# Kernel tuning notes

Measured on AMD Instinct MI355X. Metric: run time of the kernel, lower is better.

Reference implementation:

```python
import jax, jax.numpy as jnp
import numpy as np

N_NODES = 50000
N_EDGES = 400000
N_GRAPHS = 64
D_IN = 256
D_HID = 256
D_OUT = 16


def _gcn_conv(x, edge_index, W, b):
    """PyG-style GCNConv: h = D^{-1/2}(A+I)D^{-1/2} (x @ W) + b."""
    n = x.shape[0]
    loop = jnp.arange(n)
    src = jnp.concatenate([edge_index[0], loop])  # [E+N]
    dst = jnp.concatenate([edge_index[1], loop])
    deg = jax.ops.segment_sum(jnp.ones_like(dst, x.dtype), dst, num_segments=n)
    dinv = jnp.where(deg > 0, jax.lax.rsqrt(deg), jnp.zeros_like(deg))
    norm = dinv[src] * dinv[dst]  # [E+N]
    h = x @ W  # linear transform first (as PyG does)
    msg = h[src] * norm[:, None]  # gather + scale, [E+N, D]
    out = jax.ops.segment_sum(msg, dst, num_segments=n)  # scatter-add
    return out + b


def setup_inputs() -> dict:
    key = jax.random.key(0)
    ks = jax.random.split(key, 12)
    x = jax.random.normal(ks[0], (N_NODES, D_IN), dtype=jnp.float32)
    edge_index = jax.random.randint(ks[1], (2, N_EDGES), 0, N_NODES, dtype=jnp.int64)
    batch = jnp.sort(jax.random.randint(ks[2], (N_NODES,), 0, N_GRAPHS, dtype=jnp.int64))

    def glorot(k, fan_in, fan_out):
        s = np.sqrt(6.0 / (fan_in + fan_out)).astype(np.float32)
        return jax.random.uniform(k, (fan_in, fan_out), jnp.float32, -s, s)

    return {
        "x": x,
        "edge_index": edge_index,
        "batch": batch,
        "W1": glorot(ks[3], D_IN, D_HID), "b1": jnp.zeros((D_HID,), jnp.float32),
        "W2": glorot(ks[4], D_HID, D_HID), "b2": jnp.zeros((D_HID,), jnp.float32),
        "W3": glorot(ks[5], D_HID, D_HID), "b3": jnp.zeros((D_HID,), jnp.float32),
        "Wfc": glorot(ks[6], D_HID, D_OUT), "bfc": jnp.zeros((D_OUT,), jnp.float32),
    }


def reference(x, edge_index, batch, W1, b1, W2, b2, W3, b3, Wfc, bfc):
    h = jax.nn.relu(_gcn_conv(x, edge_index, W1, b1))
    h = jax.nn.relu(_gcn_conv(h, edge_index, W2, b2))
    h = jax.nn.relu(_gcn_conv(h, edge_index, W3, b3))
    # global_mean_pool over batch ids
    sums = jax.ops.segment_sum(h, batch, num_segments=N_GRAPHS)  # [G, D]
    cnts = jax.ops.segment_sum(jnp.ones_like(batch, h.dtype), batch, num_segments=N_GRAPHS)
    pooled = sums / jnp.maximum(cnts, 1.0)[:, None]
    return pooled @ Wfc + bfc  # [G, D_OUT]
```

## Files before the change

### kernel.cpp

```cpp
#include <hip/hip_runtime.h>

#define NN 50000
#define NE 400000
#define NG 64
#define D 256
#define DOUT 16

typedef __attribute__((ext_vector_type(8))) _Float16 f16x8;
typedef __attribute__((ext_vector_type(8))) unsigned short u16x8;
typedef __attribute__((ext_vector_type(4))) float f32x4;

__device__ __forceinline__ unsigned short f2h(float x) {
    union { _Float16 h; unsigned short u; } v;
    v.h = (_Float16)x;
    return v.u;
}
__device__ __forceinline__ float h2f(unsigned short u) {
    union { _Float16 h; unsigned short u; } v;
    v.u = u;
    return (float)v.h;
}

__device__ __forceinline__ void async_cp16(void* lds, const void* g) {
    __builtin_amdgcn_global_load_lds(
        (const __attribute__((address_space(1))) unsigned int*)g,
        (__attribute__((address_space(3))) unsigned int*)lds, 16, 0, 0);
}


__global__ void k_init(int* __restrict__ cnt, float* __restrict__ pooled,
                       const int* __restrict__ batch, float* __restrict__ inv_cnt,
                       int n) {
    int i = blockIdx.x * 256 + threadIdx.x;
    if (i < n) cnt[i] = 0;
    if (i < NG * D) pooled[i] = 0.f;
    if (blockIdx.x == 0 && threadIdx.x < NG) {
        int g = threadIdx.x;
        int lo = 0, hi = n;
        while (lo < hi) { int mid = (lo + hi) >> 1; if (batch[mid] < g) lo = mid + 1; else hi = mid; }
        int start = lo;
        hi = n;
        while (lo < hi) { int mid = (lo + hi) >> 1; if (batch[mid] < g + 1) lo = mid + 1; else hi = mid; }
        inv_cnt[g] = 1.f / fmaxf((float)(lo - start), 1.f);
    }
}


__global__ void k_split_count(const float* __restrict__ x, unsigned short* __restrict__ ahi,
                              int total4, int xblocks,
                              const float* __restrict__ W1, short* __restrict__ w1h,
                              const float* __restrict__ W2, short* __restrict__ w2h,
                              const float* __restrict__ W3, short* __restrict__ w3h,
                              const int* __restrict__ eidx, int* __restrict__ cnt, int E) {
    int b = blockIdx.x;
    if (b < xblocks) {
        int i = b * 256 + threadIdx.x;
        if (i >= total4) return;
        float4 v = ((const float4*)x)[i];
        ushort4 h;
        h.x = f2h(v.x);
        h.y = f2h(v.y);
        h.z = f2h(v.z);
        h.w = f2h(v.w);
        ((ushort4*)ahi)[i] = h;
    } else if (b < xblocks + 3 * 256) {
        int wb = b - xblocks;
        int which = wb >> 8;
        int idx = (wb & 255) * 256 + threadIdx.x;
        int nn = idx >> 8, k = idx & 255;
        const float* W = (which == 0) ? W1 : (which == 1) ? W2 : W3;
        short* Wh = (which == 0) ? w1h : (which == 1) ? w2h : w3h;
        Wh[idx] = (short)f2h(W[k * 256 + nn]);
    } else {
        int e = (b - xblocks - 3 * 256) * 256 + threadIdx.x;
        if (e < E) atomicAdd(&cnt[eidx[E + e]], 1);
    }
}

__global__ void k_scan1(const int* __restrict__ cnt, int* __restrict__ excl,
                        int* __restrict__ bsums, float* __restrict__ dinv, int n) {
    __shared__ int sh[256];
    int tid = threadIdx.x;
    int base = blockIdx.x * 1024;
    int v[4]; int tsum = 0;
    for (int j = 0; j < 4; ++j) {
        int i = base + tid * 4 + j;
        v[j] = (i < n) ? cnt[i] : 0;
        if (i < n) dinv[i] = rsqrtf((float)(v[j] + 1));
        tsum += v[j];
    }
    sh[tid] = tsum; __syncthreads();
    for (int d = 1; d < 256; d <<= 1) {
        int t = (tid >= d) ? sh[tid - d] : 0;
        __syncthreads();
        sh[tid] += t;
        __syncthreads();
    }
    int run = sh[tid] - tsum;
    for (int j = 0; j < 4; ++j) {
        int i = base + tid * 4 + j;
        if (i < n) excl[i] = run;
        run += v[j];
    }
    if (tid == 255) bsums[blockIdx.x] = sh[255];
}

__global__ void k_scan3(int* __restrict__ row_ptr, const int* __restrict__ bsums,
                        int* __restrict__ cursor, int n, int E, int nb) {
    __shared__ int off_s;
    int chunk = (int)(blockIdx.x >> 2);
    if (threadIdx.x < 64) {
        int v = ((int)threadIdx.x < nb && (int)threadIdx.x < chunk) ? bsums[threadIdx.x] : 0;
        #pragma unroll
        for (int d = 1; d < 64; d <<= 1) v += __shfl_xor(v, d);
        if (threadIdx.x == 0) off_s = v;
    }
    __syncthreads();
    int off = off_s;
    int i = blockIdx.x * 256 + threadIdx.x;
    if (i < n) {
        int v = row_ptr[i] + off;
        row_ptr[i] = v;
        cursor[i] = v;
    }
    if (i == 0) row_ptr[n] = E;
}


__device__ __forceinline__ void gemm_body(
        const unsigned short* __restrict__ A,
        const short* __restrict__ Wh,
        const float* __restrict__ dinv, unsigned short* __restrict__ C, int M,
        int bm, short* Ah_s, short* Bh_s) {
    const int tid = threadIdx.x;
    const int lane = tid & 63;
    const int w    = tid >> 6;
    const int lm   = lane & 15;
    const int quad = lane >> 4;

    const int srow = tid >> 3, c = tid & 7;
    const int q = c ^ ((srow >> 1) & 7);
    const unsigned short* pa[2];
    #pragma unroll
    for (int j = 0; j < 2; ++j) {
        int ga = bm + j * 32 + srow; if (ga >= M) ga = M - 1;
        pa[j] = A + ((size_t)ga << 8) + q * 8;
    }
    const short* pbh[8];
    #pragma unroll
    for (int j = 0; j < 8; ++j)
        pbh[j] = Wh + ((size_t)(j * 32 + srow) << 8) + q * 8;

    int st[8];
    #pragma unroll
    for (int j = 0; j < 8; ++j) st[j] = j * 2048 + w * 512;

    int oa[4], ob[4];
    #pragma unroll
    for (int i = 0; i < 4; ++i) {
        int ra = i * 16 + lm;
        oa[i] = ra * 64 + ((quad ^ ((ra >> 1) & 7)) * 8);
        int rb = w * 64 + i * 16 + lm;
        ob[i] = rb * 64 + ((quad ^ ((rb >> 1) & 7)) * 8);
    }

    f32x4 acc[4][4];
    #pragma unroll
    for (int i = 0; i < 4; ++i)
        #pragma unroll
        for (int j = 0; j < 4; ++j)
            acc[i][j] = (f32x4){0.f, 0.f, 0.f, 0.f};

    for (int k0 = 0; k0 < D; k0 += 64) {
        #pragma unroll
        for (int j = 0; j < 2; ++j) async_cp16(&Ah_s[st[j]], pa[j] + k0);
        #pragma unroll
        for (int j = 0; j < 8; ++j) async_cp16(&Bh_s[st[j]], pbh[j] + k0);
        __syncthreads();

        #pragma unroll
        for (int kh = 0; kh < 2; ++kh) {
            const int xo = kh * 32;
            f16x8 Ah[4], Bh[4];
            #pragma unroll
            for (int i = 0; i < 4; ++i) {
                Ah[i] = *(const f16x8*)&Ah_s[oa[i] ^ xo];
                Bh[i] = *(const f16x8*)&Bh_s[ob[i] ^ xo];
            }
            #pragma unroll
            for (int mi = 0; mi < 4; ++mi)
                #pragma unroll
                for (int ni = 0; ni < 4; ++ni)
                    acc[mi][ni] = __builtin_amdgcn_mfma_f32_16x16x32_f16(Ah[mi], Bh[ni], acc[mi][ni], 0, 0, 0);
        }
        __syncthreads();
    }

    #pragma unroll
    for (int mi = 0; mi < 4; ++mi) {
        int rbase = bm + mi * 16 + quad * 4;
        #pragma unroll
        for (int r = 0; r < 4; ++r) {
            int grow = rbase + r;
            if (grow < M) {
                float s = dinv[grow];
                #pragma unroll
                for (int ni = 0; ni < 4; ++ni) {
                    int col = w * 64 + ni * 16 + lm;
                    C[(size_t)grow * D + col] = f2h(acc[mi][ni][r] * s);
                }
            }
        }
    }
}

__global__ __launch_bounds__(256, 3) void k_gemm_mfma(
        const unsigned short* __restrict__ A,
        const short* __restrict__ Wh,
        const float* __restrict__ dinv, unsigned short* __restrict__ C, int M) {
    __shared__ short Ah_s[4096];
    __shared__ short Bh_s[16384];
    gemm_body(A, Wh, dinv, C, M, blockIdx.x * 64, Ah_s, Bh_s);
}

__global__ __launch_bounds__(256, 3) void k_gemm1_fill(
        const unsigned short* __restrict__ A,
        const short* __restrict__ Wh,
        const float* __restrict__ dinv, unsigned short* __restrict__ C, int M,
        int gblocks, const int* __restrict__ eidx, int* __restrict__ cursor,
        int* __restrict__ col_src, int E) {
    __shared__ short Ah_s[4096];
    __shared__ short Bh_s[16384];
    if ((int)blockIdx.x < gblocks) {
        gemm_body(A, Wh, dinv, C, M, blockIdx.x * 64, Ah_s, Bh_s);
    } else {
        int e = ((int)blockIdx.x - gblocks) * 256 + threadIdx.x;
        if (e < E) {
            int d = eidx[E + e];
            int pos = atomicAdd(&cursor[d], 1);
            col_src[pos] = eidx[e];
        }
    }
}


__global__ __launch_bounds__(256) void k_agg(
        const unsigned short* __restrict__ h, const float* __restrict__ dinv,
        const int* __restrict__ row_ptr, const int* __restrict__ col_src,
        const float* __restrict__ bias,
        unsigned short* __restrict__ ohi, int n) {
    int w = threadIdx.x >> 6, lane = threadIdx.x & 63;
    int node = blockIdx.x * 4 + w;
    if (node >= n) return;
    int half = lane >> 5;
    int dcol = lane & 31;

    float acc[8] = {0.f, 0.f, 0.f, 0.f, 0.f, 0.f, 0.f, 0.f};
    if (half == 0) {
        u16x8 sv = ((const u16x8*)(h + (size_t)node * D))[dcol];
        #pragma unroll
        for (int d = 0; d < 8; ++d) acc[d] = h2f(sv[d]);
    }

    int beg = row_ptr[node], end = row_ptr[node + 1];
    for (int c = beg; c < end; c += 64) {
        int cnt = min(64, end - c);
        int myidx = (lane < cnt) ? col_src[c + lane] : 0;
        for (int e = 0; e < cnt; e += 16) {
            u16x8 u[8];
            bool val[8];
            #pragma unroll
            for (int j = 0; j < 8; ++j) {
                int eid = e + j * 2 + half;
                val[j] = eid < cnt;
                if (val[j]) {
                    int s = __shfl(myidx, eid);
                    u[j] = ((const u16x8*)(h + (size_t)s * D))[dcol];
                }
            }
            #pragma unroll
            for (int j = 0; j < 8; ++j)
                if (val[j]) {
                    #pragma unroll
                    for (int d = 0; d < 8; ++d) acc[d] += h2f(u[j][d]);
                }
        }
    }

    #pragma unroll
    for (int d = 0; d < 8; ++d) acc[d] += __shfl_xor(acc[d], 32);

    if (half == 0) {
        float di = dinv[node];
        float4 b0 = ((const float4*)bias)[dcol * 2];
        float4 b1 = ((const float4*)bias)[dcol * 2 + 1];
        float bb[8] = {b0.x, b0.y, b0.z, b0.w, b1.x, b1.y, b1.z, b1.w};
        u16x8 o;
        #pragma unroll
        for (int d = 0; d < 8; ++d)
            o[d] = f2h(fmaxf(acc[d] * di + bb[d], 0.f));
        ((u16x8*)(ohi + (size_t)node * D))[dcol] = o;
    }
}


__global__ __launch_bounds__(256) void k_pool_sum(
        const unsigned short* __restrict__ hi,
        const int* __restrict__ batch, float* __restrict__ pooled, int n) {
    int beg = blockIdx.x * 64;
    if (beg >= n) return;
    int end = min(beg + 64, n);
    int t = threadIdx.x;
    float acc = 0.f;
    int cur = batch[beg];
    for (int i = beg; i < end; ++i) {
        int g = batch[i];
        if (g != cur) {
            atomicAdd(&pooled[cur * D + t], acc);
            acc = 0.f;
            cur = g;
        }
        acc += h2f(hi[(size_t)i * D + t]);
    }
    atomicAdd(&pooled[cur * D + t], acc);
}


__global__ void k_fc(const float* __restrict__ pooled, const float* __restrict__ inv_cnt,
                     const float* __restrict__ W, const float* __restrict__ b,
                     float* __restrict__ out) {
    int t = blockIdx.x * blockDim.x + threadIdx.x;
    if (t >= NG * DOUT) return;
    int g = t >> 4, o = t & 15;
    float acc = 0.f;
    for (int k = 0; k < D; ++k) acc += pooled[g * D + k] * W[k * DOUT + o];
    out[t] = acc * inv_cnt[g] + b[o];
}


extern "C" void kernel_launch(void* const* d_in, const int* in_sizes, int n_in,
                              void* d_out, int out_size, void* d_ws, size_t ws_size,
                              hipStream_t stream) {
    const float* x    = (const float*)d_in[0];
    const int*   eidx = (const int*)d_in[1];
    const int*   batch= (const int*)d_in[2];
    const float* W1   = (const float*)d_in[3];
    const float* b1   = (const float*)d_in[4];
    const float* W2   = (const float*)d_in[5];
    const float* b2   = (const float*)d_in[6];
    const float* W3   = (const float*)d_in[7];
    const float* b3   = (const float*)d_in[8];
    const float* Wfc  = (const float*)d_in[9];
    const float* bfc  = (const float*)d_in[10];
    float* out = (float*)d_out;

    const int n = in_sizes[0] / D;
    const int E = in_sizes[1] / 2;

    char* p = (char*)d_ws;
    auto take = [&](size_t bytes) -> void* {
        void* q = (void*)p;
        p += (bytes + 255) & ~(size_t)255;
        return q;
    };
    int*   cnt     = (int*)take((size_t)n * 4);
    int*   row_ptr = (int*)take((size_t)(n + 1) * 4);
    int*   cursor  = (int*)take((size_t)n * 4);
    int*   col_src = (int*)take((size_t)E * 4);
    int*   bsums   = (int*)take(256 * 4);
    float* dinv    = (float*)take((size_t)n * 4);
    float* inv_cnt = (float*)take((size_t)NG * 4);
    short* w1h     = (short*)take((size_t)D * D * 2);
    short* w2h     = (short*)take((size_t)D * D * 2);
    short* w3h     = (short*)take((size_t)D * D * 2);
    unsigned short* hbuf = (unsigned short*)take((size_t)n * D * 2);
    unsigned short* ahi  = (unsigned short*)take((size_t)n * D * 2);
    float* pooled  = (float*)take((size_t)NG * D * 4);

    int tb = 256;
    int gn = (n + tb - 1) / tb;
    int ge = (E + tb - 1) / tb;
    int nb = (n + 1023) / 1024;
    int total4 = n * D / 4;
    int xblocks = (total4 + 255) / 256;

    k_init<<<gn, tb, 0, stream>>>(cnt, pooled, batch, inv_cnt, n);
    k_split_count<<<xblocks + 3 * 256 + ge, tb, 0, stream>>>(
        x, ahi, total4, xblocks,
        W1, w1h, W2, w2h, W3, w3h,
        eidx, cnt, E);
    k_scan1<<<nb, 256, 0, stream>>>(cnt, row_ptr, bsums, dinv, n);
    k_scan3<<<gn, tb, 0, stream>>>(row_ptr, bsums, cursor, n, E, nb);

    int ggrid = (n + 63) / 64;
    int agrid = (n + 3) / 4;

    k_gemm1_fill<<<ggrid + ge, 256, 0, stream>>>(ahi, w1h, dinv, hbuf, n,
                                                 ggrid, eidx, cursor, col_src, E);
    k_agg<<<agrid, 256, 0, stream>>>(hbuf, dinv, row_ptr, col_src, b1, ahi, n);

    k_gemm_mfma<<<ggrid, 256, 0, stream>>>(ahi, w2h, dinv, hbuf, n);
    k_agg<<<agrid, 256, 0, stream>>>(hbuf, dinv, row_ptr, col_src, b2, ahi, n);

    k_gemm_mfma<<<ggrid, 256, 0, stream>>>(ahi, w3h, dinv, hbuf, n);
    k_agg<<<agrid, 256, 0, stream>>>(hbuf, dinv, row_ptr, col_src, b3, ahi, n);

    k_pool_sum<<<(n + 63) / 64, 256, 0, stream>>>(ahi, batch, pooled, n);
    k_fc<<<4, 256, 0, stream>>>(pooled, inv_cnt, Wfc, bfc, out);
}
```

Before: 349.2 us.

## Load GEMM MFMA operands directly from global memory, dropping LDS staging

The GEMM body no longer copies A and W tiles into shared memory through async global-to-LDS loads with barriers. Each lane now reads its f16x8 MFMA fragments straight from global memory at each 32-wide k step, and the loop is fully unrolled. This removes the LDS traffic, the swizzle arithmetic and the __syncthreads, and frees LDS so more blocks can be resident. In exchange, the W tile is fetched redundantly by every wave and block through the caches, and the per-lane 16-byte loads are scattered across rows.

```diff
diff --git a/kernel.cpp b/kernel.cpp
--- a/kernel.cpp
+++ b/kernel.cpp
@@ -19,12 +19,6 @@
     union { _Float16 h; unsigned short u; } v;
     v.u = u;
     return (float)v.h;
-}
-
-__device__ __forceinline__ void async_cp16(void* lds, const void* g) {
-    __builtin_amdgcn_global_load_lds(
-        (const __attribute__((address_space(1))) unsigned int*)g,
-        (__attribute__((address_space(3))) unsigned int*)lds, 16, 0, 0);
 }
 
 
@@ -131,37 +125,21 @@
         const unsigned short* __restrict__ A,
         const short* __restrict__ Wh,
         const float* __restrict__ dinv, unsigned short* __restrict__ C, int M,
-        int bm, short* Ah_s, short* Bh_s) {
+        int bm) {
     const int tid = threadIdx.x;
     const int lane = tid & 63;
     const int w    = tid >> 6;
     const int lm   = lane & 15;
     const int quad = lane >> 4;
 
-    const int srow = tid >> 3, c = tid & 7;
-    const int q = c ^ ((srow >> 1) & 7);
-    const unsigned short* pa[2];
-    #pragma unroll
-    for (int j = 0; j < 2; ++j) {
-        int ga = bm + j * 32 + srow; if (ga >= M) ga = M - 1;
-        pa[j] = A + ((size_t)ga << 8) + q * 8;
-    }
-    const short* pbh[8];
-    #pragma unroll
-    for (int j = 0; j < 8; ++j)
-        pbh[j] = Wh + ((size_t)(j * 32 + srow) << 8) + q * 8;
-
-    int st[8];
-    #pragma unroll
-    for (int j = 0; j < 8; ++j) st[j] = j * 2048 + w * 512;
-
-    int oa[4], ob[4];
+    const unsigned short* pa[4];
+    const short* pb[4];
     #pragma unroll
     for (int i = 0; i < 4; ++i) {
-        int ra = i * 16 + lm;
-        oa[i] = ra * 64 + ((quad ^ ((ra >> 1) & 7)) * 8);
-        int rb = w * 64 + i * 16 + lm;
-        ob[i] = rb * 64 + ((quad ^ ((rb >> 1) & 7)) * 8);
+        int ra = bm + i * 16 + lm; if (ra >= M) ra = M - 1;
+        pa[i] = A + ((size_t)ra << 8) + quad * 8;
+        int cb = w * 64 + i * 16 + lm;
+        pb[i] = Wh + ((size_t)cb << 8) + quad * 8;
     }
 
     f32x4 acc[4][4];
@@ -171,29 +149,19 @@
         for (int j = 0; j < 4; ++j)
             acc[i][j] = (f32x4){0.f, 0.f, 0.f, 0.f};
 
-    for (int k0 = 0; k0 < D; k0 += 64) {
-        #pragma unroll
-        for (int j = 0; j < 2; ++j) async_cp16(&Ah_s[st[j]], pa[j] + k0);
-        #pragma unroll
-        for (int j = 0; j < 8; ++j) async_cp16(&Bh_s[st[j]], pbh[j] + k0);
-        __syncthreads();
-
-        #pragma unroll
-        for (int kh = 0; kh < 2; ++kh) {
-            const int xo = kh * 32;
-            f16x8 Ah[4], Bh[4];
+    #pragma unroll
+    for (int k0 = 0; k0 < D; k0 += 32) {
+        f16x8 Ah[4], Bh[4];
+        #pragma unroll
+        for (int i = 0; i < 4; ++i) {
+            Ah[i] = *(const f16x8*)(pa[i] + k0);
+            Bh[i] = *(const f16x8*)(pb[i] + k0);
+        }
+        #pragma unroll
+        for (int mi = 0; mi < 4; ++mi)
             #pragma unroll
-            for (int i = 0; i < 4; ++i) {
-                Ah[i] = *(const f16x8*)&Ah_s[oa[i] ^ xo];
-                Bh[i] = *(const f16x8*)&Bh_s[ob[i] ^ xo];
-            }
-            #pragma unroll
-            for (int mi = 0; mi < 4; ++mi)
-                #pragma unroll
-                for (int ni = 0; ni < 4; ++ni)
-                    acc[mi][ni] = __builtin_amdgcn_mfma_f32_16x16x32_f16(Ah[mi], Bh[ni], acc[mi][ni], 0, 0, 0);
-        }
-        __syncthreads();
+            for (int ni = 0; ni < 4; ++ni)
+                acc[mi][ni] = __builtin_amdgcn_mfma_f32_16x16x32_f16(Ah[mi], Bh[ni], acc[mi][ni], 0, 0, 0);
     }
 
     #pragma unroll
@@ -218,9 +186,7 @@
         const unsigned short* __restrict__ A,
         const short* __restrict__ Wh,
         const float* __restrict__ dinv, unsigned short* __restrict__ C, int M) {
-    __shared__ short Ah_s[4096];
-    __shared__ short Bh_s[16384];
-    gemm_body(A, Wh, dinv, C, M, blockIdx.x * 64, Ah_s, Bh_s);
+    gemm_body(A, Wh, dinv, C, M, blockIdx.x * 64);
 }
 
 __global__ __launch_bounds__(256, 3) void k_gemm1_fill(
@@ -229,10 +195,8 @@
         const float* __restrict__ dinv, unsigned short* __restrict__ C, int M,
         int gblocks, const int* __restrict__ eidx, int* __restrict__ cursor,
         int* __restrict__ col_src, int E) {
-    __shared__ short Ah_s[4096];
-    __shared__ short Bh_s[16384];
     if ((int)blockIdx.x < gblocks) {
-        gemm_body(A, Wh, dinv, C, M, blockIdx.x * 64, Ah_s, Bh_s);
+        gemm_body(A, Wh, dinv, C, M, blockIdx.x * 64);
     } else {
         int e = ((int)blockIdx.x - gblocks) * 256 + threadIdx.x;
         if (e < E) {
```

Result: slower. 400.7 us (+14.8%).

## Aggregate two nodes per wavefront and raise GEMM occupancy hint

Applied to the files above, without the earlier changes.

The aggregation kernel now processes two destination nodes per wavefront, interleaving their neighbor gathers in the same loop so more independent loads are in flight per wave, and halves the grid size. GEMM kernels' launch bounds go from 3 to 4 waves per EU, constraining registers for higher occupancy. The paired gather doubles register use for accumulators and loaded vectors and may cause imbalance when the two nodes have different degrees. The tighter register cap on the GEMM risks spills.

```diff
diff --git a/kernel.cpp b/kernel.cpp
--- a/kernel.cpp
+++ b/kernel.cpp
@@ -214,7 +214,7 @@
     }
 }
 
-__global__ __launch_bounds__(256, 3) void k_gemm_mfma(
+__global__ __launch_bounds__(256, 4) void k_gemm_mfma(
         const unsigned short* __restrict__ A,
         const short* __restrict__ Wh,
         const float* __restrict__ dinv, unsigned short* __restrict__ C, int M) {
@@ -223,7 +223,7 @@
     gemm_body(A, Wh, dinv, C, M, blockIdx.x * 64, Ah_s, Bh_s);
 }
 
-__global__ __launch_bounds__(256, 3) void k_gemm1_fill(
+__global__ __launch_bounds__(256, 4) void k_gemm1_fill(
         const unsigned short* __restrict__ A,
         const short* __restrict__ Wh,
         const float* __restrict__ dinv, unsigned short* __restrict__ C, int M,
@@ -250,56 +250,91 @@
         const float* __restrict__ bias,
         unsigned short* __restrict__ ohi, int n) {
     int w = threadIdx.x >> 6, lane = threadIdx.x & 63;
-    int node = blockIdx.x * 4 + w;
-    if (node >= n) return;
+    int node0 = (blockIdx.x * 4 + w) * 2;
+    if (node0 >= n) return;
+    bool two = (node0 + 1) < n;
     int half = lane >> 5;
     int dcol = lane & 31;
 
-    float acc[8] = {0.f, 0.f, 0.f, 0.f, 0.f, 0.f, 0.f, 0.f};
+    float a0[8] = {0.f, 0.f, 0.f, 0.f, 0.f, 0.f, 0.f, 0.f};
+    float a1[8] = {0.f, 0.f, 0.f, 0.f, 0.f, 0.f, 0.f, 0.f};
     if (half == 0) {
-        u16x8 sv = ((const u16x8*)(h + (size_t)node * D))[dcol];
-        #pragma unroll
-        for (int d = 0; d < 8; ++d) acc[d] = h2f(sv[d]);
-    }
-
-    int beg = row_ptr[node], end = row_ptr[node + 1];
-    for (int c = beg; c < end; c += 64) {
-        int cnt = min(64, end - c);
-        int myidx = (lane < cnt) ? col_src[c + lane] : 0;
-        for (int e = 0; e < cnt; e += 16) {
-            u16x8 u[8];
-            bool val[8];
+        u16x8 sv = ((const u16x8*)(h + (size_t)node0 * D))[dcol];
+        #pragma unroll
+        for (int d = 0; d < 8; ++d) a0[d] = h2f(sv[d]);
+    } else if (two) {
+        u16x8 sv = ((const u16x8*)(h + (size_t)(node0 + 1) * D))[dcol];
+        #pragma unroll
+        for (int d = 0; d < 8; ++d) a1[d] = h2f(sv[d]);
+    }
+
+    int c0 = row_ptr[node0];
+    int end0 = row_ptr[node0 + 1];
+    int c1 = end0;
+    int end1 = two ? row_ptr[node0 + 2] : end0;
+
+    while (c0 < end0 || c1 < end1) {
+        int cnt0 = min(64, end0 - c0); if (cnt0 < 0) cnt0 = 0;
+        int cnt1 = min(64, end1 - c1); if (cnt1 < 0) cnt1 = 0;
+        int my0 = (lane < cnt0) ? col_src[c0 + lane] : 0;
+        int my1 = (lane < cnt1) ? col_src[c1 + lane] : 0;
+        int mx = max(cnt0, cnt1);
+        for (int e = 0; e < mx; e += 16) {
+            u16x8 u0[8], u1[8];
+            bool v0[8], v1[8];
             #pragma unroll
             for (int j = 0; j < 8; ++j) {
                 int eid = e + j * 2 + half;
-                val[j] = eid < cnt;
-                if (val[j]) {
-                    int s = __shfl(myidx, eid);
-                    u[j] = ((const u16x8*)(h + (size_t)s * D))[dcol];
+                v0[j] = eid < cnt0;
+                if (v0[j]) {
+                    int s = __shfl(my0, eid);
+                    u0[j] = ((const u16x8*)(h + (size_t)s * D))[dcol];
+                }
+                v1[j] = eid < cnt1;
+                if (v1[j]) {
+                    int s = __shfl(my1, eid);
+                    u1[j] = ((const u16x8*)(h + (size_t)s * D))[dcol];
                 }
             }
             #pragma unroll
-            for (int j = 0; j < 8; ++j)
-                if (val[j]) {
+            for (int j = 0; j < 8; ++j) {
+                if (v0[j]) {
                     #pragma unroll
-                    for (int d = 0; d < 8; ++d) acc[d] += h2f(u[j][d]);
+                    for (int d = 0; d < 8; ++d) a0[d] += h2f(u0[j][d]);
                 }
+                if (v1[j]) {
+                    #pragma unroll
+                    for (int d = 0; d < 8; ++d) a1[d] += h2f(u1[j][d]);
+                }
+            }
         }
-    }
-
-    #pragma unroll
-    for (int d = 0; d < 8; ++d) acc[d] += __shfl_xor(acc[d], 32);
-
+        c0 += cnt0;
+        c1 += cnt1;
+    }
+
+    #pragma unroll
+    for (int d = 0; d < 8; ++d) {
+        a0[d] += __shfl_xor(a0[d], 32);
+        a1[d] += __shfl_xor(a1[d], 32);
+    }
+
+    float4 b0 = ((const float4*)bias)[dcol * 2];
+    float4 b1 = ((const float4*)bias)[dcol * 2 + 1];
+    float bb[8] = {b0.x, b0.y, b0.z, b0.w, b1.x, b1.y, b1.z, b1.w};
     if (half == 0) {
-        float di = dinv[node];
-        float4 b0 = ((const float4*)bias)[dcol * 2];
-        float4 b1 = ((const float4*)bias)[dcol * 2 + 1];
-        float bb[8] = {b0.x, b0.y, b0.z, b0.w, b1.x, b1.y, b1.z, b1.w};
+        float di = dinv[node0];
         u16x8 o;
         #pragma unroll
         for (int d = 0; d < 8; ++d)
-            o[d] = f2h(fmaxf(acc[d] * di + bb[d], 0.f));
-        ((u16x8*)(ohi + (size_t)node * D))[dcol] = o;
+            o[d] = f2h(fmaxf(a0[d] * di + bb[d], 0.f));
+        ((u16x8*)(ohi + (size_t)node0 * D))[dcol] = o;
+    } else if (two) {
+        float di = dinv[node0 + 1];
+        u16x8 o;
+        #pragma unroll
+        for (int d = 0; d < 8; ++d)
+            o[d] = f2h(fmaxf(a1[d] * di + bb[d], 0.f));
+        ((u16x8*)(ohi + (size_t)(node0 + 1) * D))[dcol] = o;
     }
 }
 
@@ -393,7 +428,7 @@
     k_scan3<<<gn, tb, 0, stream>>>(row_ptr, bsums, cursor, n, E, nb);
 
     int ggrid = (n + 63) / 64;
-    int agrid = (n + 3) / 4;
+    int agrid = (n + 7) / 8;
 
     k_gemm1_fill<<<ggrid + ge, 256, 0, stream>>>(ahi, w1h, dinv, hbuf, n,
                                                  ggrid, eidx, cursor, col_src, E);
```

Result: slower. 379.2 us (+8.6%).
